# Kernel optimization log

Hardware: AMD Instinct MI355X
Metric: run time of the kernel (lower is better)

## Reference

```python
import jax, jax.numpy as jnp
import numpy as np

N = 100000        # ncount
IN_C = 128        # in_channels
OUT_C = 64        # out_channels
S = 3             # number of wavelet scales
NNZ = 1_600_000   # nonzeros per sparse wavelet matrix (avg degree 16)
NNZ_F = 1_600_000 # nonzeros in sparse feature matrix


def spmm(indices, values, n_rows, dense):
    """Sparse [n_rows, *] COO matrix times dense matrix: out[r] += v * dense[c]."""
    rows, cols = indices[0], indices[1]
    return jax.ops.segment_sum(values[:, None] * dense[cols], rows, num_segments=n_rows)


def setup_inputs() -> dict:
    key = jax.random.key(0)
    ks = jax.random.split(key, 10)
    phi_indices = jax.random.randint(ks[0], (S, 2, NNZ), 0, N)
    phi_values = jax.random.uniform(ks[1], (S, NNZ), dtype=jnp.float32) * 0.1
    phi_inverse_indices = jax.random.randint(ks[2], (S, 2, NNZ), 0, N)
    phi_inverse_values = jax.random.uniform(ks[3], (S, NNZ), dtype=jnp.float32) * 0.1
    feat_rows = jax.random.randint(ks[4], (1, NNZ_F), 0, N)
    feat_cols = jax.random.randint(ks[5], (1, NNZ_F), 0, IN_C)
    feature_indices = jnp.concatenate([feat_rows, feat_cols], axis=0)
    feature_values = jax.random.uniform(ks[6], (NNZ_F,), dtype=jnp.float32)
    # xavier_uniform for weight_matrix
    bound = float(np.sqrt(6.0 / (IN_C + OUT_C)))
    weight_matrix = jax.random.uniform(ks[7], (IN_C, OUT_C), minval=-bound, maxval=bound, dtype=jnp.float32)
    # uniform(0.9, 1.1) diagonal filter (Theta)
    diagonal_weight_filter = jax.random.uniform(ks[8], (N, 1), minval=0.9, maxval=1.1, dtype=jnp.float32)
    return {
        'phi_indices': phi_indices,
        'phi_values': phi_values,
        'phi_inverse_indices': phi_inverse_indices,
        'phi_inverse_values': phi_inverse_values,
        'feature_indices': feature_indices,
        'feature_values': feature_values,
        'weight_matrix': weight_matrix,
        'diagonal_weight_filter': diagonal_weight_filter,
        'dropout': 0,  # eval mode: dropout is identity
    }


def reference(phi_indices, phi_values, phi_inverse_indices, phi_inverse_values,
              feature_indices, feature_values, weight_matrix, diagonal_weight_filter,
              dropout):
    # filtered = (sparse features) @ W   : [N, OUT_C]
    filtered = spmm(feature_indices, feature_values, N, weight_matrix)
    theta = diagonal_weight_filter[:, 0]  # [N]
    # Per scale: (phi @ diag(theta) @ phi_inv) @ filtered
    #          = phi @ (theta * (phi_inv @ filtered))   -- same math, no [N,N] product
    outs = []
    for i in range(S):  # fixed small number of scales
        z = spmm(phi_inverse_indices[i], phi_inverse_values[i], N, filtered)  # [N, OUT_C]
        z = theta[:, None] * z
        outs.append(spmm(phi_indices[i], phi_values[i], N, z))
    localized = jnp.stack(outs, axis=1)  # [N, S, OUT_C]
    # relu then dropout (eval: identity)
    return jax.nn.relu(localized)
```

## Files before the change

### kernel.cpp

```cpp
#include <hip/hip_runtime.h>
#include <hip/hip_bf16.h>

#define N_ROWS 100000
#define IN_C   128
#define OUT_C  64
#define S_SC   3
#define NNZ    1600000
#define NMAT   7
#define NCOL   8

#define SEG       512
#define BLKS_SCAN 196

#define NSEG   (NNZ / 256)
#define RPB    25000
#define NBIN_H 4

#define RPB_F  1024
#define NBKT   98
#define EPB_A  2048
#define BLKS_A ((NNZ + EPB_A - 1) / EPB_A)
#define RS_STR (N_ROWS + 1)

struct RowPtrs { const int* p[NMAT]; };

__device__ __forceinline__ float bf2f(__hip_bfloat16 x) { return __bfloat162float(x); }

__global__ __launch_bounds__(512)
void hist_binned(RowPtrs P, int* __restrict__ counts8)
{
    __shared__ unsigned cnt[RPB / 2];
    const int m    = blockIdx.y;
    const int c    = blockIdx.x & 7;
    const int bin0 = (blockIdx.x >> 3) * RPB;
    const int t    = threadIdx.x;

    for (int i = t; i < RPB / 2; i += 512) cnt[i] = 0;
    __syncthreads();

    const int* rows = P.p[m];
    const int wv = t >> 6;
    const int ln = t & 63;

    for (int sg = c + 8 * wv; sg < NSEG; sg += 64) {
        const int4 v = ((const int4*)rows)[sg * 64 + ln];
        unsigned i0 = (unsigned)(v.x - bin0);
        unsigned i1 = (unsigned)(v.y - bin0);
        unsigned i2 = (unsigned)(v.z - bin0);
        unsigned i3 = (unsigned)(v.w - bin0);
        if (i0 < RPB) atomicAdd(&cnt[i0 >> 1], 1u << ((i0 & 1) * 16));
        if (i1 < RPB) atomicAdd(&cnt[i1 >> 1], 1u << ((i1 & 1) * 16));
        if (i2 < RPB) atomicAdd(&cnt[i2 >> 1], 1u << ((i2 & 1) * 16));
        if (i3 < RPB) atomicAdd(&cnt[i3 >> 1], 1u << ((i3 & 1) * 16));
    }
    __syncthreads();

    int* dst = counts8 + ((size_t)m * NCOL + c) * N_ROWS + bin0;
    for (int i = t; i < RPB / 2; i += 512) {
        const unsigned w = cnt[i];
        ((int2*)dst)[i] = make_int2((int)(w & 0xffffu), (int)(w >> 16));
    }
}

__global__ __launch_bounds__(256)
void scan_l1(const int* __restrict__ counts8, int* __restrict__ rs,
             int* __restrict__ bsum)
{
    __shared__ int buf[2][SEG];
    const int m   = blockIdx.y;
    const int blk = blockIdx.x;
    const int t   = threadIdx.x;
    const int* cnt = counts8 + (size_t)m * NCOL * N_ROWS;

    for (int k = t; k < SEG; k += 256) {
        const int g = blk * SEG + k;
        int tot = 0;
        if (g < N_ROWS)
            for (int c = 0; c < NCOL; ++c) tot += cnt[c * N_ROWS + g];
        buf[0][k] = tot;
    }
    __syncthreads();

    int src = 0;
    for (int off = 1; off < SEG; off <<= 1) {
        for (int k = t; k < SEG; k += 256) {
            int v = buf[src][k];
            if (k >= off) v += buf[src][k - off];
            buf[1 - src][k] = v;
        }
        src ^= 1;
        __syncthreads();
    }
    for (int k = t; k < SEG; k += 256) {
        const int g = blk * SEG + k;
        if (g < N_ROWS)
            rs[(size_t)m * RS_STR + g] = (k == 0) ? 0 : buf[src][k - 1];
    }
    if (t == 0) bsum[m * 256 + blk] = buf[src][SEG - 1];
}

__global__ __launch_bounds__(256)
void scan_l2(int* __restrict__ bsum)
{
    __shared__ int buf[2][256];
    const int t = threadIdx.x;
    int* b = bsum + blockIdx.x * 256;
    buf[0][t] = (t < BLKS_SCAN) ? b[t] : 0;
    __syncthreads();
    int src = 0;
    for (int off = 1; off < 256; off <<= 1) {
        int v = buf[src][t];
        if (t >= off) v += buf[src][t - off];
        buf[1 - src][t] = v;
        src ^= 1;
        __syncthreads();
    }
    if (t < BLKS_SCAN) b[t] = (t == 0) ? 0 : buf[src][t - 1];
}

__global__ __launch_bounds__(256)
void finalize(const int* __restrict__ bsum, int* __restrict__ rs,
              int* __restrict__ bucket_cur)
{
    const int i = blockIdx.x * 256 + threadIdx.x;
    if (i >= NMAT * N_ROWS) return;
    const int m = i / N_ROWS;
    const int r = i - m * N_ROWS;
    const size_t ri = (size_t)m * RS_STR + r;
    const int base = rs[ri] + bsum[m * 256 + r / SEG];
    rs[ri] = base;
    if ((r & (RPB_F - 1)) == 0) bucket_cur[m * NBKT + (r >> 10)] = base;
    if (r == 0) rs[(size_t)m * RS_STR + N_ROWS] = NNZ;
}

__global__ __launch_bounds__(256)
void fill_a(const int* __restrict__ rows, const int* __restrict__ cols,
            const float* __restrict__ vals, int* __restrict__ bcur,
            uint2* __restrict__ bkt)
{
    __shared__ int cnt[NBKT], lofs[NBKT], lcur[NBKT], gbase[NBKT];
    __shared__ uint2 stg[EPB_A];
    __shared__ int gpos[EPB_A];
    const int t  = threadIdx.x;
    const int e0 = blockIdx.x * EPB_A;
    const int n  = min(EPB_A, NNZ - e0);

    for (int b = t; b < NBKT; b += 256) cnt[b] = 0;
    __syncthreads();

    int rr[8], cc[8], bb[8]; unsigned vv[8];
    #pragma unroll
    for (int k = 0; k < 8; ++k) {
        const int idx = t + k * 256;
        if (idx < n) {
            const int e = e0 + idx;
            rr[k] = rows[e];
            cc[k] = cols[e];
            vv[k] = __float_as_uint(vals[e]);
            bb[k] = rr[k] >> 10;
            atomicAdd(&cnt[bb[k]], 1);
        } else bb[k] = -1;
    }
    __syncthreads();

    if (t == 0) {
        int run = 0;
        for (int b = 0; b < NBKT; ++b) { lofs[b] = run; run += cnt[b]; }
    }
    __syncthreads();
    if (t < NBKT) {
        gbase[t] = atomicAdd(&bcur[t], cnt[t]);
        lcur[t]  = lofs[t];
    }
    __syncthreads();

    #pragma unroll
    for (int k = 0; k < 8; ++k) {
        if (bb[k] >= 0) {
            const int p = atomicAdd(&lcur[bb[k]], 1);
            stg[p]  = make_uint2(((unsigned)(rr[k] & (RPB_F - 1)) << 17) |
                                 (unsigned)cc[k], vv[k]);
            gpos[p] = gbase[bb[k]] + (p - lofs[bb[k]]);
        }
    }
    __syncthreads();

    for (int p = t; p < n; p += 256)
        bkt[gpos[p]] = stg[p];
}

__global__ __launch_bounds__(256)
void fill_b(const int* __restrict__ rs, const uint2* __restrict__ bkt,
            uint2* __restrict__ scv)
{
    __shared__ int cur[RPB_F];
    const int b  = blockIdx.x;
    const int r0 = b << 10;
    const int nr = min(RPB_F, N_ROWS - r0);
    const int t  = threadIdx.x;

    for (int i = t; i < nr; i += 256) cur[i] = rs[r0 + i];
    __syncthreads();

    const int e0 = rs[r0];
    const int e1 = rs[min(r0 + RPB_F, N_ROWS)];
    for (int e = e0 + t; e < e1; e += 256) {
        const uint2 rec = bkt[e];
        const int rl = (int)(rec.x >> 17);
        const int p  = atomicAdd(&cur[rl], 1);
        scv[p] = make_uint2(rec.x & 0x1FFFFu, rec.y);
    }
}

__global__ __launch_bounds__(256)
void gather_W(const int* __restrict__ rs, const uint2* __restrict__ scv,
              const float* __restrict__ W, __hip_bfloat16* __restrict__ dst)
{
    __shared__ float Wl[IN_C * OUT_C];
    for (int i = threadIdx.x; i < IN_C * OUT_C; i += blockDim.x) Wl[i] = W[i];
    __syncthreads();

    const int lane = threadIdx.x & 63;
    const int wave = blockIdx.x * 4 + (threadIdx.x >> 6);
    const int nw   = gridDim.x * 4;

    for (int r = wave; r < N_ROWS; r += nw) {
        const int s = rs[r], t = rs[r + 1];
        float a0 = 0.f, a1 = 0.f, a2 = 0.f, a3 = 0.f;
        int j = s;
        for (; j + 3 < t; j += 4) {
            const uint2 p0 = scv[j],     p1 = scv[j + 1];
            const uint2 p2 = scv[j + 2], p3 = scv[j + 3];
            a0 += __uint_as_float(p0.y) * Wl[p0.x * OUT_C + lane];
            a1 += __uint_as_float(p1.y) * Wl[p1.x * OUT_C + lane];
            a2 += __uint_as_float(p2.y) * Wl[p2.x * OUT_C + lane];
            a3 += __uint_as_float(p3.y) * Wl[p3.x * OUT_C + lane];
        }
        for (; j < t; ++j) {
            const uint2 p = scv[j];
            a0 += __uint_as_float(p.y) * Wl[p.x * OUT_C + lane];
        }
        dst[r * OUT_C + lane] = __float2bfloat16((a0 + a1) + (a2 + a3));
    }
}

template <int MODE>
__global__ __launch_bounds__(256)
void gather_mat(const int* __restrict__ rs, const uint2* __restrict__ scv,
                const __hip_bfloat16* __restrict__ src,
                const float* __restrict__ theta,
                __hip_bfloat16* __restrict__ dstb,
                float* __restrict__ dstf, int scale)
{
    const int lane = threadIdx.x & 63;
    const int wave = blockIdx.x * 4 + (threadIdx.x >> 6);
    const int nw   = gridDim.x * 4;

    for (int r = wave; r < N_ROWS; r += nw) {
        const int s = rs[r], t = rs[r + 1];
        float a0 = 0.f, a1 = 0.f, a2 = 0.f, a3 = 0.f;
        int j = s;
        for (; j + 3 < t; j += 4) {
            const uint2 p0 = scv[j],     p1 = scv[j + 1];
            const uint2 p2 = scv[j + 2], p3 = scv[j + 3];
            const float w0 = bf2f(src[p0.x * OUT_C + lane]);
            const float w1 = bf2f(src[p1.x * OUT_C + lane]);
            const float w2 = bf2f(src[p2.x * OUT_C + lane]);
            const float w3 = bf2f(src[p3.x * OUT_C + lane]);
            a0 += __uint_as_float(p0.y) * w0;
            a1 += __uint_as_float(p1.y) * w1;
            a2 += __uint_as_float(p2.y) * w2;
            a3 += __uint_as_float(p3.y) * w3;
        }
        for (; j < t; ++j) {
            const uint2 p = scv[j];
            a0 += __uint_as_float(p.y) * bf2f(src[p.x * OUT_C + lane]);
        }
        const float acc = (a0 + a1) + (a2 + a3);
        if (MODE == 1) {
            dstb[r * OUT_C + lane] = __float2bfloat16(theta[r] * acc);
        } else {
            dstf[(r * S_SC + scale) * OUT_C + lane] = acc > 0.0f ? acc : 0.0f;
        }
    }
}

extern "C" void kernel_launch(void* const* d_in, const int* in_sizes, int n_in,
                              void* d_out, int out_size, void* d_ws, size_t ws_size,
                              hipStream_t stream)
{
    const int*   phi_idx  = (const int*)d_in[0];
    const float* phi_val  = (const float*)d_in[1];
    const int*   pinv_idx = (const int*)d_in[2];
    const float* pinv_val = (const float*)d_in[3];
    const int*   fidx     = (const int*)d_in[4];
    const float* fval     = (const float*)d_in[5];
    const float* W        = (const float*)d_in[6];
    const float* theta    = (const float*)d_in[7];
    float*       out      = (float*)d_out;

    __hip_bfloat16* filtered = (__hip_bfloat16*)d_ws;
    __hip_bfloat16* z        = filtered + (size_t)N_ROWS * OUT_C;
    uint2* bkt = (uint2*)(z + (size_t)N_ROWS * OUT_C);
    uint2* scv = bkt + NNZ;
    int*   counts8    = (int*)(scv + NNZ);
    int*   rs         = counts8 + (size_t)NMAT * NCOL * N_ROWS;
    int*   bsum       = rs + (size_t)NMAT * RS_STR;
    int*   bucket_cur = bsum + NMAT * 256;

    RowPtrs P;
    P.p[0] = fidx;
    for (int i = 0; i < S_SC; ++i) {
        P.p[1 + 2 * i] = pinv_idx + (size_t)(2 * i) * NNZ;
        P.p[2 + 2 * i] = phi_idx  + (size_t)(2 * i) * NNZ;
    }

    hist_binned<<<dim3(NCOL * NBIN_H, NMAT), 512, 0, stream>>>(P, counts8);
    scan_l1<<<dim3(BLKS_SCAN, NMAT), 256, 0, stream>>>(counts8, rs, bsum);
    scan_l2<<<NMAT, 256, 0, stream>>>(bsum);
    finalize<<<(NMAT * N_ROWS + 255) / 256, 256, 0, stream>>>(bsum, rs, bucket_cur);

    fill_a<<<BLKS_A, 256, 0, stream>>>(fidx, fidx + NNZ, fval, bucket_cur, bkt);
    fill_b<<<NBKT, 256, 0, stream>>>(rs, bkt, scv);
    gather_W<<<2048, 256, 0, stream>>>(rs, scv, W, filtered);

    for (int i = 0; i < S_SC; ++i) {
        const int m1 = 1 + 2 * i, m2 = 2 + 2 * i;
        const int*   zc = pinv_idx + (size_t)(2 * i + 1) * NNZ;
        const float* zv = pinv_val + (size_t)i * NNZ;
        const int*   oc = phi_idx  + (size_t)(2 * i + 1) * NNZ;
        const float* ov = phi_val  + (size_t)i * NNZ;

        fill_a<<<BLKS_A, 256, 0, stream>>>(P.p[m1], zc, zv,
                                           bucket_cur + m1 * NBKT, bkt);
        fill_b<<<NBKT, 256, 0, stream>>>(rs + (size_t)m1 * RS_STR, bkt, scv);
        gather_mat<1><<<4096, 256, 0, stream>>>(rs + (size_t)m1 * RS_STR, scv,
                                                filtered, theta, z, nullptr, 0);

        fill_a<<<BLKS_A, 256, 0, stream>>>(P.p[m2], oc, ov,
                                           bucket_cur + m2 * NBKT, bkt);
        fill_b<<<NBKT, 256, 0, stream>>>(rs + (size_t)m2 * RS_STR, bkt, scv);
        gather_mat<2><<<4096, 256, 0, stream>>>(rs + (size_t)m2 * RS_STR, scv,
                                                z, nullptr, nullptr, out, i);
    }
}
```

Before: 1.109 ms.

## Process row pairs per wave with readlane broadcast, finer buckets and packed histograms

```diff
diff --git a/kernel.cpp b/kernel.cpp
--- a/kernel.cpp
+++ b/kernel.cpp
@@ -7,7 +7,9 @@
 #define S_SC   3
 #define NNZ    1600000
 #define NMAT   7
-#define NCOL   8
+
+#define NCH    16
+#define HROWS  (N_ROWS / 2)
 
 #define SEG       512
 #define BLKS_SCAN 196
@@ -16,8 +18,8 @@
 #define RPB    25000
 #define NBIN_H 4
 
-#define RPB_F  1024
-#define NBKT   98
+#define RPB_F  256
+#define NBKT   391
 #define EPB_A  2048
 #define BLKS_A ((NNZ + EPB_A - 1) / EPB_A)
 #define RS_STR (N_ROWS + 1)
@@ -25,14 +27,17 @@
 struct RowPtrs { const int* p[NMAT]; };
 
 __device__ __forceinline__ float bf2f(__hip_bfloat16 x) { return __bfloat162float(x); }
+__device__ __forceinline__ unsigned rdlane(unsigned v, int l) {
+    return (unsigned)__builtin_amdgcn_readlane((int)v, l);
+}
 
 __global__ __launch_bounds__(512)
-void hist_binned(RowPtrs P, int* __restrict__ counts8)
+void hist_binned(RowPtrs P, unsigned* __restrict__ counts16)
 {
     __shared__ unsigned cnt[RPB / 2];
     const int m    = blockIdx.y;
-    const int c    = blockIdx.x & 7;
-    const int bin0 = (blockIdx.x >> 3) * RPB;
+    const int c    = blockIdx.x & (NCH - 1);
+    const int bin0 = (blockIdx.x >> 4) * RPB;
     const int t    = threadIdx.x;
 
     for (int i = t; i < RPB / 2; i += 512) cnt[i] = 0;
@@ -42,7 +47,7 @@
     const int wv = t >> 6;
     const int ln = t & 63;
 
-    for (int sg = c + 8 * wv; sg < NSEG; sg += 64) {
+    for (int sg = c + NCH * wv; sg < NSEG; sg += NCH * 8) {
         const int4 v = ((const int4*)rows)[sg * 64 + ln];
         unsigned i0 = (unsigned)(v.x - bin0);
         unsigned i1 = (unsigned)(v.y - bin0);
@@ -55,28 +60,28 @@
     }
     __syncthreads();
 
-    int* dst = counts8 + ((size_t)m * NCOL + c) * N_ROWS + bin0;
-    for (int i = t; i < RPB / 2; i += 512) {
-        const unsigned w = cnt[i];
-        ((int2*)dst)[i] = make_int2((int)(w & 0xffffu), (int)(w >> 16));
-    }
-}
-
-__global__ __launch_bounds__(256)
-void scan_l1(const int* __restrict__ counts8, int* __restrict__ rs,
+    unsigned* dst = counts16 + ((size_t)m * NCH + c) * HROWS + (bin0 >> 1);
+    for (int i = t; i < RPB / 2; i += 512) dst[i] = cnt[i];
+}
+
+__global__ __launch_bounds__(256)
+void scan_l1(const unsigned* __restrict__ counts16, int* __restrict__ rs,
              int* __restrict__ bsum)
 {
     __shared__ int buf[2][SEG];
     const int m   = blockIdx.y;
     const int blk = blockIdx.x;
     const int t   = threadIdx.x;
-    const int* cnt = counts8 + (size_t)m * NCOL * N_ROWS;
+    const unsigned* cnt = counts16 + (size_t)m * NCH * HROWS;
 
     for (int k = t; k < SEG; k += 256) {
         const int g = blk * SEG + k;
         int tot = 0;
-        if (g < N_ROWS)
-            for (int c = 0; c < NCOL; ++c) tot += cnt[c * N_ROWS + g];
+        if (g < N_ROWS) {
+            const int wi = g >> 1, sh = (g & 1) * 16;
+            for (int c = 0; c < NCH; ++c)
+                tot += (int)((cnt[(size_t)c * HROWS + wi] >> sh) & 0xffffu);
+        }
         buf[0][k] = tot;
     }
     __syncthreads();
@@ -129,7 +134,7 @@
     const size_t ri = (size_t)m * RS_STR + r;
     const int base = rs[ri] + bsum[m * 256 + r / SEG];
     rs[ri] = base;
-    if ((r & (RPB_F - 1)) == 0) bucket_cur[m * NBKT + (r >> 10)] = base;
+    if ((r & (RPB_F - 1)) == 0) bucket_cur[m * NBKT + (r >> 8)] = base;
     if (r == 0) rs[(size_t)m * RS_STR + N_ROWS] = NNZ;
 }
 
@@ -141,6 +146,7 @@
     __shared__ int cnt[NBKT], lofs[NBKT], lcur[NBKT], gbase[NBKT];
     __shared__ uint2 stg[EPB_A];
     __shared__ int gpos[EPB_A];
+    __shared__ int ps[2][256];
     const int t  = threadIdx.x;
     const int e0 = blockIdx.x * EPB_A;
     const int n  = min(EPB_A, NNZ - e0);
@@ -157,21 +163,38 @@
             rr[k] = rows[e];
             cc[k] = cols[e];
             vv[k] = __float_as_uint(vals[e]);
-            bb[k] = rr[k] >> 10;
+            bb[k] = rr[k] >> 8;
             atomicAdd(&cnt[bb[k]], 1);
         } else bb[k] = -1;
     }
     __syncthreads();
 
-    if (t == 0) {
-        int run = 0;
-        for (int b = 0; b < NBKT; ++b) { lofs[b] = run; run += cnt[b]; }
-    }
-    __syncthreads();
-    if (t < NBKT) {
-        gbase[t] = atomicAdd(&bcur[t], cnt[t]);
-        lcur[t]  = lofs[t];
-    }
+    {
+        int v[4]; int s = 0;
+        #pragma unroll
+        for (int k = 0; k < 4; ++k) {
+            const int b = 4 * t + k;
+            v[k] = (b < NBKT) ? cnt[b] : 0; s += v[k];
+        }
+        ps[0][t] = s;
+        __syncthreads();
+        int sp = 0;
+        for (int off = 1; off < 256; off <<= 1) {
+            ps[1 - sp][t] = ps[sp][t] + ((t >= off) ? ps[sp][t - off] : 0);
+            sp ^= 1;
+            __syncthreads();
+        }
+        int base = (t == 0) ? 0 : ps[sp][t - 1];
+        #pragma unroll
+        for (int k = 0; k < 4; ++k) {
+            const int b = 4 * t + k;
+            if (b < NBKT) { lofs[b] = base; lcur[b] = base; base += v[k]; }
+        }
+    }
+    __syncthreads();
+
+    for (int b = t; b < NBKT; b += 256)
+        gbase[b] = atomicAdd(&bcur[b], cnt[b]);
     __syncthreads();
 
     #pragma unroll
@@ -185,8 +208,7 @@
     }
     __syncthreads();
 
-    for (int p = t; p < n; p += 256)
-        bkt[gpos[p]] = stg[p];
+    for (int p = t; p < n; p += 256) bkt[gpos[p]] = stg[p];
 }
 
 __global__ __launch_bounds__(256)
@@ -195,7 +217,7 @@
 {
     __shared__ int cur[RPB_F];
     const int b  = blockIdx.x;
-    const int r0 = b << 10;
+    const int r0 = b << 8;
     const int nr = min(RPB_F, N_ROWS - r0);
     const int t  = threadIdx.x;
 
@@ -224,23 +246,39 @@
     const int wave = blockIdx.x * 4 + (threadIdx.x >> 6);
     const int nw   = gridDim.x * 4;
 
-    for (int r = wave; r < N_ROWS; r += nw) {
-        const int s = rs[r], t = rs[r + 1];
-        float a0 = 0.f, a1 = 0.f, a2 = 0.f, a3 = 0.f;
-        int j = s;
-        for (; j + 3 < t; j += 4) {
-            const uint2 p0 = scv[j],     p1 = scv[j + 1];
-            const uint2 p2 = scv[j + 2], p3 = scv[j + 3];
-            a0 += __uint_as_float(p0.y) * Wl[p0.x * OUT_C + lane];
-            a1 += __uint_as_float(p1.y) * Wl[p1.x * OUT_C + lane];
-            a2 += __uint_as_float(p2.y) * Wl[p2.x * OUT_C + lane];
-            a3 += __uint_as_float(p3.y) * Wl[p3.x * OUT_C + lane];
-        }
-        for (; j < t; ++j) {
-            const uint2 p = scv[j];
-            a0 += __uint_as_float(p.y) * Wl[p.x * OUT_C + lane];
-        }
-        dst[r * OUT_C + lane] = __float2bfloat16((a0 + a1) + (a2 + a3));
+    for (int p = wave; p < N_ROWS / 2; p += nw) {
+        const int rA = 2 * p;
+        const int sA = rs[rA], tA = rs[rA + 1], tB = rs[rA + 2];
+        const int lenA = tA - sA, lenB = tB - tA, len = tB - sA;
+        float aA = 0.f, aB = 0.f;
+        if (len <= 64) {
+            uint2 q = make_uint2(0u, 0u);
+            if (lane < len) q = scv[sA + lane];
+            const int mx = (lenA > lenB) ? lenA : lenB;
+            for (int k = 0; k < mx; ++k) {
+                if (k < lenA) {
+                    const unsigned c = rdlane(q.x, k);
+                    const unsigned v = rdlane(q.y, k);
+                    aA += __uint_as_float(v) * Wl[c * OUT_C + lane];
+                }
+                if (k < lenB) {
+                    const unsigned c = rdlane(q.x, lenA + k);
+                    const unsigned v = rdlane(q.y, lenA + k);
+                    aB += __uint_as_float(v) * Wl[c * OUT_C + lane];
+                }
+            }
+        } else {
+            for (int j = sA; j < tA; ++j) {
+                const uint2 q = scv[j];
+                aA += __uint_as_float(q.y) * Wl[q.x * OUT_C + lane];
+            }
+            for (int j = tA; j < tB; ++j) {
+                const uint2 q = scv[j];
+                aB += __uint_as_float(q.y) * Wl[q.x * OUT_C + lane];
+            }
+        }
+        dst[(size_t)rA * OUT_C + lane]       = __float2bfloat16(aA);
+        dst[(size_t)(rA + 1) * OUT_C + lane] = __float2bfloat16(aB);
     }
 }
 
@@ -256,31 +294,43 @@
     const int wave = blockIdx.x * 4 + (threadIdx.x >> 6);
     const int nw   = gridDim.x * 4;
 
-    for (int r = wave; r < N_ROWS; r += nw) {
-        const int s = rs[r], t = rs[r + 1];
-        float a0 = 0.f, a1 = 0.f, a2 = 0.f, a3 = 0.f;
-        int j = s;
-        for (; j + 3 < t; j += 4) {
-            const uint2 p0 = scv[j],     p1 = scv[j + 1];
-            const uint2 p2 = scv[j + 2], p3 = scv[j + 3];
-            const float w0 = bf2f(src[p0.x * OUT_C + lane]);
-            const float w1 = bf2f(src[p1.x * OUT_C + lane]);
-            const float w2 = bf2f(src[p2.x * OUT_C + lane]);
-            const float w3 = bf2f(src[p3.x * OUT_C + lane]);
-            a0 += __uint_as_float(p0.y) * w0;
-            a1 += __uint_as_float(p1.y) * w1;
-            a2 += __uint_as_float(p2.y) * w2;
-            a3 += __uint_as_float(p3.y) * w3;
-        }
-        for (; j < t; ++j) {
-            const uint2 p = scv[j];
-            a0 += __uint_as_float(p.y) * bf2f(src[p.x * OUT_C + lane]);
-        }
-        const float acc = (a0 + a1) + (a2 + a3);
+    for (int p = wave; p < N_ROWS / 2; p += nw) {
+        const int rA = 2 * p;
+        const int sA = rs[rA], tA = rs[rA + 1], tB = rs[rA + 2];
+        const int lenA = tA - sA, lenB = tB - tA, len = tB - sA;
+        float aA = 0.f, aB = 0.f;
+        if (len <= 64) {
+            uint2 q = make_uint2(0u, 0u);
+            if (lane < len) q = scv[sA + lane];
+            const int mx = (lenA > lenB) ? lenA : lenB;
+            for (int k = 0; k < mx; ++k) {
+                if (k < lenA) {
+                    const unsigned c = rdlane(q.x, k);
+                    const unsigned v = rdlane(q.y, k);
+                    aA += __uint_as_float(v) * bf2f(src[(size_t)c * OUT_C + lane]);
+                }
+                if (k < lenB) {
+                    const unsigned c = rdlane(q.x, lenA + k);
+                    const unsigned v = rdlane(q.y, lenA + k);
+                    aB += __uint_as_float(v) * bf2f(src[(size_t)c * OUT_C + lane]);
+                }
+            }
+        } else {
+            for (int j = sA; j < tA; ++j) {
+                const uint2 q = scv[j];
+                aA += __uint_as_float(q.y) * bf2f(src[(size_t)q.x * OUT_C + lane]);
+            }
+            for (int j = tA; j < tB; ++j) {
+                const uint2 q = scv[j];
+                aB += __uint_as_float(q.y) * bf2f(src[(size_t)q.x * OUT_C + lane]);
+            }
+        }
         if (MODE == 1) {
-            dstb[r * OUT_C + lane] = __float2bfloat16(theta[r] * acc);
+            dstb[(size_t)rA * OUT_C + lane]       = __float2bfloat16(theta[rA] * aA);
+            dstb[(size_t)(rA + 1) * OUT_C + lane] = __float2bfloat16(theta[rA + 1] * aB);
         } else {
-            dstf[(r * S_SC + scale) * OUT_C + lane] = acc > 0.0f ? acc : 0.0f;
+            dstf[((size_t)rA * S_SC + scale) * OUT_C + lane]       = aA > 0.f ? aA : 0.f;
+            dstf[((size_t)(rA + 1) * S_SC + scale) * OUT_C + lane] = aB > 0.f ? aB : 0.f;
         }
     }
 }
@@ -303,10 +353,10 @@
     __hip_bfloat16* z        = filtered + (size_t)N_ROWS * OUT_C;
     uint2* bkt = (uint2*)(z + (size_t)N_ROWS * OUT_C);
     uint2* scv = bkt + NNZ;
-    int*   counts8    = (int*)(scv + NNZ);
-    int*   rs         = counts8 + (size_t)NMAT * NCOL * N_ROWS;
-    int*   bsum       = rs + (size_t)NMAT * RS_STR;
-    int*   bucket_cur = bsum + NMAT * 256;
+    unsigned* counts16 = (unsigned*)(scv + NNZ);
+    int*   rs          = (int*)(counts16 + (size_t)NMAT * NCH * HROWS);
+    int*   bsum        = rs + (size_t)NMAT * RS_STR;
+    int*   bucket_cur  = bsum + NMAT * 256;
 
     RowPtrs P;
     P.p[0] = fidx;
@@ -315,14 +365,14 @@
         P.p[2 + 2 * i] = phi_idx  + (size_t)(2 * i) * NNZ;
     }
 
-    hist_binned<<<dim3(NCOL * NBIN_H, NMAT), 512, 0, stream>>>(P, counts8);
-    scan_l1<<<dim3(BLKS_SCAN, NMAT), 256, 0, stream>>>(counts8, rs, bsum);
+    hist_binned<<<dim3(NCH * NBIN_H, NMAT), 512, 0, stream>>>(P, counts16);
+    scan_l1<<<dim3(BLKS_SCAN, NMAT), 256, 0, stream>>>(counts16, rs, bsum);
     scan_l2<<<NMAT, 256, 0, stream>>>(bsum);
     finalize<<<(NMAT * N_ROWS + 255) / 256, 256, 0, stream>>>(bsum, rs, bucket_cur);
 
     fill_a<<<BLKS_A, 256, 0, stream>>>(fidx, fidx + NNZ, fval, bucket_cur, bkt);
     fill_b<<<NBKT, 256, 0, stream>>>(rs, bkt, scv);
-    gather_W<<<2048, 256, 0, stream>>>(rs, scv, W, filtered);
+    gather_W<<<4096, 256, 0, stream>>>(rs, scv, W, filtered);
 
     for (int i = 0; i < S_SC; ++i) {
         const int m1 = 1 + 2 * i, m2 = 2 + 2 * i;
```

Measured after the change: 1.192 ms. 7.5% more time.
